# Optimization experiments

Measured on AMD Instinct MI355X. Metric: run time of the kernel, lower is better.

The kernel has to match this reference:

```python
import jax, jax.numpy as jnp
import numpy as np

NUM_EDGES = 10000
NUM_PATHS = 30000
MAX_LEN = 16
LINK_DIM = 128
PATH_DIM = 128


def setup_inputs() -> dict:
    key = jax.random.key(0)
    k0, k1, k2, k3, k4, k5, k6, k7 = jax.random.split(key, 8)
    inputs = jax.random.normal(k0, (NUM_EDGES, LINK_DIM), dtype=jnp.float32)
    # every path has exactly MAX_LEN hops -> unique (path, pos) scatter indices
    idx = jnp.repeat(jnp.arange(NUM_PATHS, dtype=jnp.int64), MAX_LEN)
    seqs = jnp.tile(jnp.arange(MAX_LEN, dtype=jnp.int64), NUM_PATHS)
    paths = jax.random.randint(k1, (NUM_PATHS * MAX_LEN,), 0, NUM_EDGES).astype(jnp.int64)
    # GRU params (Keras GRUCell, reset_after=True): kernel [D,3U], recurrent [U,3U], two bias rows
    s_in = 1.0 / np.sqrt(LINK_DIM)
    s_h = 1.0 / np.sqrt(PATH_DIM)
    kernel = jax.random.uniform(k2, (LINK_DIM, 3 * PATH_DIM), minval=-s_in, maxval=s_in, dtype=jnp.float32)
    rec_kernel = jax.random.uniform(k3, (PATH_DIM, 3 * PATH_DIM), minval=-s_h, maxval=s_h, dtype=jnp.float32)
    bias_i = jnp.zeros((3 * PATH_DIM,), dtype=jnp.float32)
    bias_r = jnp.zeros((3 * PATH_DIM,), dtype=jnp.float32)
    wq = jax.random.uniform(k4, (PATH_DIM, PATH_DIM), minval=-s_h, maxval=s_h, dtype=jnp.float32)
    wk = jax.random.uniform(k5, (PATH_DIM, PATH_DIM), minval=-s_h, maxval=s_h, dtype=jnp.float32)
    wv = jax.random.uniform(k6, (PATH_DIM, PATH_DIM), minval=-s_h, maxval=s_h, dtype=jnp.float32)
    return {"inputs": inputs, "paths": paths, "idx": idx, "seqs": seqs,
            "kernel": kernel, "rec_kernel": rec_kernel, "bias_i": bias_i, "bias_r": bias_r,
            "wq": wq, "wk": wk, "wv": wv}


def _gru_scan(link_inputs, kernel, rec_kernel, bias_i, bias_r):
    # link_inputs: [P, L, D] -> hidden_states [P, L, U], last_state [P, U]
    U = rec_kernel.shape[0]
    P = link_inputs.shape[0]
    xs = jnp.transpose(link_inputs, (1, 0, 2))  # [L, P, D]

    def step(h, x):
        xm = x @ kernel + bias_i          # [P, 3U]
        hm = h @ rec_kernel + bias_r      # [P, 3U]  (reset_after=True)
        xz, xr, xh = xm[:, :U], xm[:, U:2 * U], xm[:, 2 * U:]
        hz, hr, hh = hm[:, :U], hm[:, U:2 * U], hm[:, 2 * U:]
        z = jax.nn.sigmoid(xz + hz)
        r = jax.nn.sigmoid(xr + hr)
        cand = jnp.tanh(xh + r * hh)
        h_new = z * h + (1.0 - z) * cand
        return h_new, h_new

    h0 = jnp.zeros((P, U), dtype=link_inputs.dtype)
    last, hs = jax.lax.scan(step, h0, xs)
    return jnp.transpose(hs, (1, 0, 2)), last  # [P, L, U], [P, U]


def reference(inputs, paths, idx, seqs, kernel, rec_kernel, bias_i, bias_r, wq, wk, wv):
    h_tild = inputs[paths]  # gather: [P*L, D]
    link_inputs = jnp.zeros((NUM_PATHS, MAX_LEN, LINK_DIM), dtype=inputs.dtype)
    link_inputs = link_inputs.at[idx, seqs].set(h_tild)  # scatter_nd
    hidden_states, last_state = _gru_scan(link_inputs, kernel, rec_kernel, bias_i, bias_r)
    key = jnp.einsum('plu,uv->plv', hidden_states, wk)
    query = last_state @ wq                     # [P, U]
    value = jnp.einsum('plu,uv->plv', hidden_states, wv)
    att = jnp.einsum('plv,pv->pl', key, query)  # raw scores, no softmax (faithful)
    context = jnp.einsum('pl,plv->pv', att, value)[:, None, :]  # [P, 1, U]
    return context
```

## Files before the change

### kernel.cpp

```cpp
#include <hip/hip_runtime.h>


#define NUM_PATHS 30000
#define T 16
#define NTILES 1875
#define NEDGES 10000

typedef float f32x4 __attribute__((ext_vector_type(4)));
typedef short bf16x8 __attribute__((ext_vector_type(8)));
typedef short bf16x4 __attribute__((ext_vector_type(4)));

__device__ __forceinline__ short f2bf(float f) {
    union { float f; unsigned u; } v; v.f = f;
    return (short)((v.u + 0x8000u) >> 16);
}
__device__ __forceinline__ float bf2f(short s) {
    union { unsigned u; float f; } v; v.u = ((unsigned)(unsigned short)s) << 16;
    return v.f;
}
__device__ __forceinline__ float fsig(float x) {
    return __builtin_amdgcn_rcpf(1.0f + __expf(-x));
}
__device__ __forceinline__ float ftanhf_(float x) {
    return 1.0f - 2.0f * __builtin_amdgcn_rcpf(1.0f + __expf(2.0f * x));
}

#define MFMA(a, b, c) __builtin_amdgcn_mfma_f32_16x16x32_bf16((a), (b), (c), 0, 0, 0)

#define GRU_T 12288
#define QK_T 16384
#define WV_T 2048
__global__ void prep_kernel(const float* __restrict__ Wx, const float* __restrict__ Wr,
                            const float* __restrict__ wq, const float* __restrict__ wk,
                            const float* __restrict__ wv,
                            short* __restrict__ wpk) {
    int id = blockIdx.x * 256 + threadIdx.x;
    if (id < GRU_T) {
        int f = id >> 9, rem = id & 511;
        int w = rem >> 6, lane = rem & 63;
        int quad = lane >> 4, c16 = lane & 15;
        int col = 16 * w + c16;
        short o[8];
        #pragma unroll
        for (int j = 0; j < 8; ++j) {
            float v;
            if (f < 16) {
                int k = (f & 7) * 32 + quad * 8 + j;
                int cc = col + ((f < 8) ? 0 : 128);
                v = (k < 128) ? Wx[k * 384 + cc] : Wr[(k - 128) * 384 + cc];
            } else {
                int k = ((f - 16) & 3) * 32 + quad * 8 + j;
                v = (f < 20) ? Wx[k * 384 + 256 + col] : Wr[k * 384 + 256 + col];
            }
            o[j] = f2bf(v);
        }
        *(bf16x8*)&wpk[id * 8] = *(bf16x8*)o;
        return;
    }
    if (id < GRU_T + QK_T) {
        int t2 = id - GRU_T;
        int j = t2 & 7, lane = (t2 >> 3) & 63, w = (t2 >> 9) & 7, kc = t2 >> 12;
        int quad = lane >> 4, c16 = lane & 15, col = 16 * w + c16;
        int k = kc * 32 + quad * 8 + j;
        const float* qr = wq + k * 128;
        const float* kr = wk + col * 128;
        float s = 0.f;
        #pragma unroll 8
        for (int vv = 0; vv < 128; ++vv) s += qr[vv] * kr[vv];
        short hi = f2bf(s);
        wpk[(((24 + kc) * 8 + w) * 64 + lane) * 8 + j] = hi;
        wpk[(((28 + kc) * 8 + w) * 64 + lane) * 8 + j] = f2bf(s - bf2f(hi));
        return;
    }
    if (id < GRU_T + QK_T + WV_T) {
        int t2 = id - GRU_T - QK_T;
        int lane = t2 & 63, w = (t2 >> 6) & 7, kc = t2 >> 9;
        int quad = lane >> 4, c16 = lane & 15, col = 16 * w + c16;
        short hi8[8], lo8[8];
        #pragma unroll
        for (int j = 0; j < 8; ++j) {
            float v = wv[(kc * 32 + quad * 8 + j) * 128 + col];
            hi8[j] = f2bf(v);
            lo8[j] = f2bf(v - bf2f(hi8[j]));
        }
        *(bf16x8*)&wpk[(((32 + kc) * 8 + w) * 64 + lane) * 8] = *(bf16x8*)hi8;
        *(bf16x8*)&wpk[(((36 + kc) * 8 + w) * 64 + lane) * 8] = *(bf16x8*)lo8;
    }
}

__global__ __launch_bounds__(512) void eprep_kernel(
    const float* __restrict__ inputs, const short* __restrict__ wpk,
    const float* __restrict__ bias_i, uint2* __restrict__ E8) {
    const int w = threadIdx.x >> 6, lane = threadIdx.x & 63;
    const int quad = lane >> 4, c16 = lane & 15;
    const int ucol = 16 * w + c16;
    const int e0 = blockIdx.x * 16;

    const float bxh = bias_i[256 + ucol];

    bf16x8 A[4];
    const float* row = inputs + (e0 + c16) * 128;
    #pragma unroll
    for (int kc = 0; kc < 4; ++kc) {
        float4 a = *(const float4*)&row[kc * 32 + quad * 8];
        float4 b = *(const float4*)&row[kc * 32 + quad * 8 + 4];
        short o[8] = {f2bf(a.x), f2bf(a.y), f2bf(a.z), f2bf(a.w),
                      f2bf(b.x), f2bf(b.y), f2bf(b.z), f2bf(b.w)};
        A[kc] = *(bf16x8*)o;
    }
    f32x4 az = {0.f, 0.f, 0.f, 0.f}, ar = az, ax = az;
    #pragma unroll
    for (int kc = 0; kc < 4; ++kc) {
        bf16x8 Bz = *(const bf16x8*)&wpk[(((0 + kc) * 8 + w) * 64 + lane) * 8];
        bf16x8 Br = *(const bf16x8*)&wpk[(((8 + kc) * 8 + w) * 64 + lane) * 8];
        bf16x8 Bx = *(const bf16x8*)&wpk[(((16 + kc) * 8 + w) * 64 + lane) * 8];
        az = MFMA(A[kc], Bz, az);
        ar = MFMA(A[kc], Br, ar);
        ax = MFMA(A[kc], Bx, ax);
    }
    #pragma unroll
    for (int r = 0; r < 4; ++r) {
        unsigned zr = (unsigned)(unsigned short)f2bf(az[r]) |
                      ((unsigned)(unsigned short)f2bf(ar[r]) << 16);
        uint2 val;
        val.x = zr;
        val.y = __float_as_uint(ax[r] + bxh);
        E8[(e0 + quad * 4 + r) * 128 + ucol] = val;
    }
}

#define ROWS 136
#define HSLOT 2184

__global__ __launch_bounds__(512, 4) void path_emb_kernel(
    const int* __restrict__ paths, const short* __restrict__ wpk,
    const uint2* __restrict__ E8,
    const float* __restrict__ bias_i, const float* __restrict__ bias_r,
    float* __restrict__ out)
{
    __shared__ __align__(16) short s_hist[16][HSLOT];
    __shared__ __align__(16) short s_xb[2][T * ROWS];
    __shared__ float s_att[2][16][20];

    const int tid  = threadIdx.x;
    const int w    = tid >> 6;
    const int lane = tid & 63;
    const int quad = lane >> 4;
    const int c16  = lane & 15;
    const int ucol = 16 * w + c16;

    const float bz  = bias_i[ucol] + bias_r[ucol];
    const float brr = bias_i[128 + ucol] + bias_r[128 + ucol];
    const float bhh = bias_r[256 + ucol];

    bf16x8 Bzh[4], Brh[4], Bhh[4];
    #pragma unroll
    for (int kc = 0; kc < 4; ++kc) {
        Bzh[kc] = *(const bf16x8*)&wpk[(((4 + kc)  * 8 + w) * 64 + lane) * 8];
        Brh[kc] = *(const bf16x8*)&wpk[(((12 + kc) * 8 + w) * 64 + lane) * 8];
        Bhh[kc] = *(const bf16x8*)&wpk[(((20 + kc) * 8 + w) * 64 + lane) * 8];
    }

    const int p0 = blockIdx.x * T;

    float hA[4] = {0.f, 0.f, 0.f, 0.f};

    const int* pbase = paths + (p0 + quad * 4) * 16;
    const uint2* Erow = E8 + ucol;

    uint2 Ea[4], Eb[4], Ec[4];

    {
        int id0[4], id1[4];
        #pragma unroll
        for (int i = 0; i < 4; ++i) id0[i] = pbase[i * 16 + 0];
        #pragma unroll
        for (int i = 0; i < 4; ++i) id1[i] = pbase[i * 16 + 1];
        #pragma unroll
        for (int i = 0; i < 4; ++i) Ea[i] = Erow[id0[i] * 128];
        #pragma unroll
        for (int i = 0; i < 4; ++i) Eb[i] = Erow[id1[i] * 128];
    }

    auto window = [&](int t, uint2* Ecur, uint2* Enxt) {
        __syncthreads();

        if (t < 14) {
            int en[4];
            #pragma unroll
            for (int i = 0; i < 4; ++i)
                en[i] = pbase[i * 16 + t + 2];
            #pragma unroll
            for (int i = 0; i < 4; ++i) Enxt[i] = Erow[en[i] * 128];
        }

        f32x4 az  = {bz, bz, bz, bz};
        f32x4 ar  = {brr, brr, brr, brr};
        f32x4 ach = {bhh, bhh, bhh, bhh};

        if (t > 0) {
            bf16x8 ah[4];
            #pragma unroll
            for (int kc = 0; kc < 4; ++kc)
                ah[kc] = *(const bf16x8*)&s_hist[t - 1][c16 * ROWS + kc * 32 + quad * 8];
            #pragma unroll
            for (int kc = 0; kc < 4; ++kc) {
                az  = MFMA(ah[kc], Bzh[kc], az);
                ar  = MFMA(ah[kc], Brh[kc], ar);
                ach = MFMA(ah[kc], Bhh[kc], ach);
            }
        }

        #pragma unroll
        for (int r = 0; r < 4; ++r) {
            uint2 Ec_ = Ecur[r];
            float zx = __uint_as_float(Ec_.x << 16);
            float rx = __uint_as_float(Ec_.x & 0xffff0000u);
            float xh = __uint_as_float(Ec_.y);
            float z    = fsig(az[r] + zx);
            float rr   = fsig(ar[r] + rx);
            float cand = ftanhf_(xh + rr * ach[r]);
            hA[r] = cand + z * (hA[r] - cand);
            s_hist[t][(quad * 4 + r) * ROWS + ucol] = f2bf(hA[r]);
        }
    };

    #pragma unroll 1
    for (int t3 = 0; t3 < 5; ++t3) {
        window(3 * t3 + 0, Ea, Ec);
        window(3 * t3 + 1, Eb, Ea);
        window(3 * t3 + 2, Ec, Eb);
    }
    window(15, Ea, Ec);

    #pragma unroll
    for (int r = 0; r < 4; ++r) {
        float hf = hA[r]; short hi = f2bf(hf);
        s_xb[0][(quad * 4 + r) * ROWS + ucol] = f2bf(hf - bf2f(hi));
    }
    __syncthreads();

    f32x4 uA = {0.f, 0.f, 0.f, 0.f};
    #pragma unroll
    for (int kc = 0; kc < 4; ++kc) {
        bf16x8 bqh = *(const bf16x8*)&wpk[(((24 + kc) * 8 + w) * 64 + lane) * 8];
        bf16x8 bql = *(const bf16x8*)&wpk[(((28 + kc) * 8 + w) * 64 + lane) * 8];
        bf16x8 Ah  = *(const bf16x8*)&s_hist[15][c16 * ROWS + kc * 32 + quad * 8];
        bf16x8 Al  = *(const bf16x8*)&s_xb[0][c16 * ROWS + kc * 32 + quad * 8];
        uA = MFMA(Ah, bqh, uA); uA = MFMA(Ah, bql, uA); uA = MFMA(Al, bqh, uA);
    }
    __syncthreads();

    #pragma unroll
    for (int r = 0; r < 4; ++r) {
        int off = (quad * 4 + r) * ROWS + ucol;
        float v = uA[r]; short hi = f2bf(v);
        s_xb[0][off] = hi; s_xb[1][off] = f2bf(v - bf2f(hi));
    }
    __syncthreads();

    {
        int half = tid >> 8, p = (tid >> 4) & 15, l = tid & 15;
        const short* uh = &s_xb[0][p * ROWS + half * 64];
        const short* ul = &s_xb[1][p * ROWS + half * 64];
        const short* hh = &s_hist[l][p * ROWS + half * 64];
        float a = 0.f;
        #pragma unroll
        for (int u8 = 0; u8 < 64; u8 += 8) {
            bf16x8 vh = *(const bf16x8*)&uh[u8];
            bf16x8 vl = *(const bf16x8*)&ul[u8];
            bf16x8 vt = *(const bf16x8*)&hh[u8];
            #pragma unroll
            for (int j = 0; j < 8; ++j)
                a += (bf2f(vh[j]) + bf2f(vl[j])) * bf2f(vt[j]);
        }
        s_att[half][p][l] = a;
    }
    __syncthreads();

    {
        int p = tid >> 5, c0 = (tid & 31) * 4;
        float ctx[4] = {0.f, 0.f, 0.f, 0.f};
        #pragma unroll
        for (int l = 0; l < 16; ++l) {
            float al = s_att[0][p][l] + s_att[1][p][l];
            bf16x4 hv = *(const bf16x4*)&s_hist[l][p * ROWS + c0];
            #pragma unroll
            for (int j = 0; j < 4; ++j) ctx[j] += al * bf2f(hv[j]);
        }
        #pragma unroll
        for (int j = 0; j < 4; ++j) {
            short hi = f2bf(ctx[j]);
            s_xb[0][p * ROWS + c0 + j] = hi;
            s_xb[1][p * ROWS + c0 + j] = f2bf(ctx[j] - bf2f(hi));
        }
    }
    __syncthreads();

    f32x4 oA = {0.f, 0.f, 0.f, 0.f};
    #pragma unroll
    for (int kc = 0; kc < 4; ++kc) {
        bf16x8 bwh = *(const bf16x8*)&wpk[(((32 + kc) * 8 + w) * 64 + lane) * 8];
        bf16x8 bwl = *(const bf16x8*)&wpk[(((36 + kc) * 8 + w) * 64 + lane) * 8];
        bf16x8 Ah  = *(const bf16x8*)&s_xb[0][c16 * ROWS + kc * 32 + quad * 8];
        bf16x8 Al  = *(const bf16x8*)&s_xb[1][c16 * ROWS + kc * 32 + quad * 8];
        oA = MFMA(Ah, bwh, oA); oA = MFMA(Ah, bwl, oA); oA = MFMA(Al, bwh, oA);
    }
    #pragma unroll
    for (int r = 0; r < 4; ++r)
        out[(p0 + quad * 4 + r) * 128 + ucol] = oA[r];
}

extern "C" void kernel_launch(void* const* d_in, const int* in_sizes, int n_in,
                              void* d_out, int out_size, void* d_ws, size_t ws_size,
                              hipStream_t stream) {
    const float* inputs = (const float*)d_in[0];
    const int*   paths  = (const int*)d_in[1];
    const float* wx  = (const float*)d_in[4];
    const float* wr  = (const float*)d_in[5];
    const float* bi  = (const float*)d_in[6];
    const float* br  = (const float*)d_in[7];
    const float* wq  = (const float*)d_in[8];
    const float* wk  = (const float*)d_in[9];
    const float* wvp = (const float*)d_in[10];

    char* ws = (char*)d_ws;
    uint2* E8 = (uint2*)ws;
    short* wpk = (short*)(ws + 10240000);

    int prep_n = GRU_T + QK_T + WV_T;
    prep_kernel<<<(prep_n + 255) / 256, 256, 0, stream>>>(wx, wr, wq, wk, wvp, wpk);
    eprep_kernel<<<NEDGES / 16, 512, 0, stream>>>(inputs, wpk, bi, E8);
    path_emb_kernel<<<NTILES, 512, 0, stream>>>(paths, wpk, E8, bi, br, (float*)d_out);
}
```

Baseline: 200.6 us.

## Fold exp2 scaling into GRU weights, prioritize MFMA, compute attention scores via MFMA

The GRU gate weights and biases are prescaled by log2(e) (and 2*log2(e) for the candidate), so the sigmoid and tanh can use raw v_exp_f32 through inline asm with no per-element multiply. The recurrent MFMA block is wrapped in s_setprio to raise wave priority while it issues. The scalar attention-score dot products are replaced by MFMA on the hidden history, with the diagonal pulled out per lane, which removes the two-half partial-sum buffer. The cost is wasted MFMA work on off-diagonal results, plus extra rounding because the weights are scaled before conversion to bf16.

```diff
diff --git a/kernel.cpp b/kernel.cpp
--- a/kernel.cpp
+++ b/kernel.cpp
@@ -6,6 +6,9 @@
 #define NTILES 1875
 #define NEDGES 10000
 
+#define SC1 1.4426950408889634f
+#define SC2 2.8853900817779268f
+
 typedef float f32x4 __attribute__((ext_vector_type(4)));
 typedef short bf16x8 __attribute__((ext_vector_type(8)));
 typedef short bf16x4 __attribute__((ext_vector_type(4)));
@@ -18,11 +21,11 @@
     union { unsigned u; float f; } v; v.u = ((unsigned)(unsigned short)s) << 16;
     return v.f;
 }
-__device__ __forceinline__ float fsig(float x) {
-    return __builtin_amdgcn_rcpf(1.0f + __expf(-x));
-}
-__device__ __forceinline__ float ftanhf_(float x) {
-    return 1.0f - 2.0f * __builtin_amdgcn_rcpf(1.0f + __expf(2.0f * x));
+__device__ __forceinline__ float vexp2(float x) {
+    float r; asm("v_exp_f32 %0, %1" : "=v"(r) : "v"(x)); return r;
+}
+__device__ __forceinline__ float vexp2n(float x) {
+    float r; asm("v_exp_f32 %0, -%1" : "=v"(r) : "v"(x)); return r;
 }
 
 #define MFMA(a, b, c) __builtin_amdgcn_mfma_f32_16x16x32_bf16((a), (b), (c), 0, 0, 0)
@@ -47,10 +50,10 @@
             if (f < 16) {
                 int k = (f & 7) * 32 + quad * 8 + j;
                 int cc = col + ((f < 8) ? 0 : 128);
-                v = (k < 128) ? Wx[k * 384 + cc] : Wr[(k - 128) * 384 + cc];
+                v = ((k < 128) ? Wx[k * 384 + cc] : Wr[(k - 128) * 384 + cc]) * SC1;
             } else {
                 int k = ((f - 16) & 3) * 32 + quad * 8 + j;
-                v = (f < 20) ? Wx[k * 384 + 256 + col] : Wr[k * 384 + 256 + col];
+                v = ((f < 20) ? Wx[k * 384 + 256 + col] : Wr[k * 384 + 256 + col]) * SC2;
             }
             o[j] = f2bf(v);
         }
@@ -96,7 +99,7 @@
     const int ucol = 16 * w + c16;
     const int e0 = blockIdx.x * 16;
 
-    const float bxh = bias_i[256 + ucol];
+    const float bxh = bias_i[256 + ucol] * SC2;
 
     bf16x8 A[4];
     const float* row = inputs + (e0 + c16) * 128;
@@ -140,7 +143,7 @@
 {
     __shared__ __align__(16) short s_hist[16][HSLOT];
     __shared__ __align__(16) short s_xb[2][T * ROWS];
-    __shared__ float s_att[2][16][20];
+    __shared__ float s_att[16][20];
 
     const int tid  = threadIdx.x;
     const int w    = tid >> 6;
@@ -149,9 +152,9 @@
     const int c16  = lane & 15;
     const int ucol = 16 * w + c16;
 
-    const float bz  = bias_i[ucol] + bias_r[ucol];
-    const float brr = bias_i[128 + ucol] + bias_r[128 + ucol];
-    const float bhh = bias_r[256 + ucol];
+    const float bz  = (bias_i[ucol] + bias_r[ucol]) * SC1;
+    const float brr = (bias_i[128 + ucol] + bias_r[128 + ucol]) * SC1;
+    const float bhh = bias_r[256 + ucol] * SC2;
 
     bf16x8 Bzh[4], Brh[4], Bhh[4];
     #pragma unroll
@@ -203,12 +206,14 @@
             #pragma unroll
             for (int kc = 0; kc < 4; ++kc)
                 ah[kc] = *(const bf16x8*)&s_hist[t - 1][c16 * ROWS + kc * 32 + quad * 8];
+            __builtin_amdgcn_s_setprio(1);
             #pragma unroll
             for (int kc = 0; kc < 4; ++kc) {
                 az  = MFMA(ah[kc], Bzh[kc], az);
                 ar  = MFMA(ah[kc], Brh[kc], ar);
                 ach = MFMA(ah[kc], Bhh[kc], ach);
             }
+            __builtin_amdgcn_s_setprio(0);
         }
 
         #pragma unroll
@@ -217,9 +222,10 @@
             float zx = __uint_as_float(Ec_.x << 16);
             float rx = __uint_as_float(Ec_.x & 0xffff0000u);
             float xh = __uint_as_float(Ec_.y);
-            float z    = fsig(az[r] + zx);
-            float rr   = fsig(ar[r] + rx);
-            float cand = ftanhf_(xh + rr * ach[r]);
+            float z    = __builtin_amdgcn_rcpf(1.0f + vexp2n(az[r] + zx));
+            float rr   = __builtin_amdgcn_rcpf(1.0f + vexp2n(ar[r] + rx));
+            float e2   = vexp2(xh + rr * ach[r]);
+            float cand = 1.0f - 2.0f * __builtin_amdgcn_rcpf(1.0f + e2);
             hA[r] = cand + z * (hA[r] - cand);
             s_hist[t][(quad * 4 + r) * ROWS + ucol] = f2bf(hA[r]);
         }
@@ -260,21 +266,27 @@
     __syncthreads();
 
     {
-        int half = tid >> 8, p = (tid >> 4) & 15, l = tid & 15;
-        const short* uh = &s_xb[0][p * ROWS + half * 64];
-        const short* ul = &s_xb[1][p * ROWS + half * 64];
-        const short* hh = &s_hist[l][p * ROWS + half * 64];
-        float a = 0.f;
-        #pragma unroll
-        for (int u8 = 0; u8 < 64; u8 += 8) {
-            bf16x8 vh = *(const bf16x8*)&uh[u8];
-            bf16x8 vl = *(const bf16x8*)&ul[u8];
-            bf16x8 vt = *(const bf16x8*)&hh[u8];
-            #pragma unroll
-            for (int j = 0; j < 8; ++j)
-                a += (bf2f(vh[j]) + bf2f(vl[j])) * bf2f(vt[j]);
-        }
-        s_att[half][p][l] = a;
+        bf16x8 Uh[4], Ul[4];
+        #pragma unroll
+        for (int kc = 0; kc < 4; ++kc) {
+            Uh[kc] = *(const bf16x8*)&s_xb[0][c16 * ROWS + kc * 32 + quad * 8];
+            Ul[kc] = *(const bf16x8*)&s_xb[1][c16 * ROWS + kc * 32 + quad * 8];
+        }
+        #pragma unroll
+        for (int li = 0; li < 2; ++li) {
+            int l = 2 * w + li;
+            f32x4 acc = {0.f, 0.f, 0.f, 0.f};
+            #pragma unroll
+            for (int kc = 0; kc < 4; ++kc) {
+                bf16x8 Bh = *(const bf16x8*)&s_hist[l][c16 * ROWS + kc * 32 + quad * 8];
+                acc = MFMA(Uh[kc], Bh, acc);
+                acc = MFMA(Ul[kc], Bh, acc);
+            }
+            float d01 = (c16 & 1) ? acc[1] : acc[0];
+            float d23 = (c16 & 1) ? acc[3] : acc[2];
+            float dv  = (c16 & 2) ? d23 : d01;
+            if (quad == (c16 >> 2)) s_att[c16][l] = dv;
+        }
     }
     __syncthreads();
 
@@ -283,7 +295,7 @@
         float ctx[4] = {0.f, 0.f, 0.f, 0.f};
         #pragma unroll
         for (int l = 0; l < 16; ++l) {
-            float al = s_att[0][p][l] + s_att[1][p][l];
+            float al = s_att[p][l];
             bf16x4 hv = *(const bf16x4*)&s_hist[l][p * ROWS + c0];
             #pragma unroll
             for (int j = 0; j < 4; ++j) ctx[j] += al * bf2f(hv[j]);
```

Result: faster. 193.7 us (-3.4%).
